# Performance work log

Measured on AMD Instinct MI355X. Metric: run time of the kernel, lower is better.

## Reference

```python
import jax, jax.numpy as jnp
import numpy as np
from jax import lax


def setup_inputs() -> dict:
    key = jax.random.key(0)
    k1, k2 = jax.random.split(key)
    L, B, d = 2048, 16, 1024
    x = jax.random.normal(k1, (L, B, d), dtype=jnp.float32)
    val_range = (3.0 / d) ** 0.5
    weight = jax.random.uniform(k2, (d, 3 * d), dtype=jnp.float32,
                                minval=-val_range, maxval=val_range)
    bias = jnp.zeros((2 * d,), dtype=jnp.float32)
    c0 = jnp.zeros((B, d), dtype=jnp.float32)
    return {"x": x, "weight": weight, "bias": bias, "c0": c0}


def reference(x, weight, bias, c0):
    # x: [L, B, d]; weight: [d, 3d]; bias: [2d]; c0: [B, d]
    L, B, d = x.shape
    u = (x.reshape(-1, d) @ weight).reshape(L, B, d, 3)
    x_tilde = u[..., 0]                               # [L, B, d]
    forget = jax.nn.sigmoid(u[..., 1] + bias[:d])     # [L, B, d]
    reset = jax.nn.sigmoid(u[..., 2] + bias[d:])      # [L, B, d]
    # k == 3 case: x_prime is the raw input (highway connection)
    x_prime = x

    def step(c_prev, ft_xt):
        ft, xt = ft_xt
        c = (c_prev - xt) * ft + xt
        return c, c

    c_last, cs = lax.scan(step, c0, (forget, x_tilde))
    g = jnp.tanh(cs)  # activation_type == 1
    h = (g - x_prime) * reset + x_prime
    return h, c_last
```

## Files before the change

kernel.cpp:

```cpp
#include <hip/hip_runtime.h>

#define L_SEQ 2048
#define BATCH 16
#define DDIM  1024
#define MDIM  (L_SEQ * BATCH)
#define NDIM  (3 * DDIM)
#define KDIM  DDIM
#define CH    (BATCH * DDIM)
#define NSEG  32
#define SEGL  64

typedef __attribute__((ext_vector_type(8))) short short8;
typedef __attribute__((ext_vector_type(4))) float f32x4;

static __device__ __forceinline__ unsigned short f2bf(float f) {
  unsigned int u = __builtin_bit_cast(unsigned int, f);
  unsigned int lsb = (u >> 16) & 1u;
  u += 0x7fffu + lsb;
  return (unsigned short)(u >> 16);
}
static __device__ __forceinline__ float bf2f(unsigned short s) {
  unsigned int u = ((unsigned int)s) << 16;
  return __builtin_bit_cast(float, u);
}

static __device__ __forceinline__ void gll16(const void* g, void* l) {
  __builtin_amdgcn_global_load_lds(
      (const __attribute__((address_space(1))) unsigned int*)g,
      (__attribute__((address_space(3))) unsigned int*)l, 16, 0, 0);
}


__global__ void k_convert_x(const float4* __restrict__ x, ushort4* __restrict__ xb, int n4) {
  int i = blockIdx.x * blockDim.x + threadIdx.x;
  int stride = gridDim.x * blockDim.x;
  for (; i < n4; i += stride) {
    float4 v = x[i];
    ushort4 o;
    o.x = f2bf(v.x); o.y = f2bf(v.y); o.z = f2bf(v.z); o.w = f2bf(v.w);
    xb[i] = o;
  }
}

__global__ void k_convert_w(const float* __restrict__ w, unsigned short* __restrict__ wb) {
  int gid = blockIdx.x * 256 + threadIdx.x;
  int k = gid & (KDIM - 1);
  int n = gid >> 10;
  int col = (n < DDIM) ? 3 * n : (n < 2 * DDIM) ? 3 * (n - DDIM) + 1 : 3 * (n - 2 * DDIM) + 2;
  wb[gid] = f2bf(w[(size_t)k * NDIM + col]);
}


#define MFMA1(I, J, A, B) \
  acc[I][J] = __builtin_amdgcn_mfma_f32_16x16x32_bf16(A, B, acc[I][J], 0, 0, 0);

#define MFMAQ(BASE)                                   \
  MFMA1(BASE + 0, 0, aa0, bb0) MFMA1(BASE + 0, 1, aa0, bb1) \
  MFMA1(BASE + 0, 2, aa0, bb2) MFMA1(BASE + 0, 3, aa0, bb3) \
  MFMA1(BASE + 1, 0, aa1, bb0) MFMA1(BASE + 1, 1, aa1, bb1) \
  MFMA1(BASE + 1, 2, aa1, bb2) MFMA1(BASE + 1, 3, aa1, bb3) \
  MFMA1(BASE + 2, 0, aa2, bb0) MFMA1(BASE + 2, 1, aa2, bb1) \
  MFMA1(BASE + 2, 2, aa2, bb2) MFMA1(BASE + 2, 3, aa2, bb3) \
  MFMA1(BASE + 3, 0, aa3, bb0) MFMA1(BASE + 3, 1, aa3, bb1) \
  MFMA1(BASE + 3, 2, aa3, bb2) MFMA1(BASE + 3, 3, aa3, bb3)

#define PH_BAR() __builtin_amdgcn_s_barrier()

#define VM_WAIT4() asm volatile("s_waitcnt vmcnt(4)" ::: "memory")

#define TILE64(T) do {                                                        \
  const char* bufC = LDSc + ((T) & 1) * 65536;                                \
  char*       bufN = LDSc + (((T) + 1) & 1) * 65536;                          \
  const int stA = (((T) + 1) & 15) * 128;                                     \
                 \
  aa0 = *(const short8*)(bufC + aRd);                                         \
  aa1 = *(const short8*)(bufC + aRd + 1024);                                  \
  aa2 = *(const short8*)(bufC + aRd + 2048);                                  \
  aa3 = *(const short8*)(bufC + aRd + 3072);                                  \
  bb0 = *(const short8*)(bufC + 32768 + bRd);                                 \
  bb1 = *(const short8*)(bufC + 32768 + bRd + 1024);                          \
  bb2 = *(const short8*)(bufC + 32768 + bRd + 2048);                          \
  bb3 = *(const short8*)(bufC + 32768 + bRd + 3072);                          \
  gll16(srcA0 + stA, bufN + dstOff);                                          \
  gll16(srcA1 + stA, bufN + 8192 + dstOff);                                   \
  PH_BAR();                                                                   \
  __builtin_amdgcn_s_setprio(1); MFMAQ(0) __builtin_amdgcn_s_setprio(0);      \
  PH_BAR();                                                                   \
              \
  aa0 = *(const short8*)(bufC + aRd + 4096);                                  \
  aa1 = *(const short8*)(bufC + aRd + 5120);                                  \
  aa2 = *(const short8*)(bufC + aRd + 6144);                                  \
  aa3 = *(const short8*)(bufC + aRd + 7168);                                  \
  gll16(srcB0 + stA, bufN + 32768 + dstOff);                                  \
  gll16(srcB1 + stA, bufN + 40960 + dstOff);                                  \
  PH_BAR();                                                                   \
  __builtin_amdgcn_s_setprio(1); MFMAQ(4) __builtin_amdgcn_s_setprio(0);      \
  VM_WAIT4();                                                                 \
  PH_BAR();                                                                   \
                 \
  aa0 = *(const short8*)(bufC + 16384 + aRd);                                 \
  aa1 = *(const short8*)(bufC + 16384 + aRd + 1024);                          \
  aa2 = *(const short8*)(bufC + 16384 + aRd + 2048);                          \
  aa3 = *(const short8*)(bufC + 16384 + aRd + 3072);                          \
  bb0 = *(const short8*)(bufC + 49152 + bRd);                                 \
  bb1 = *(const short8*)(bufC + 49152 + bRd + 1024);                          \
  bb2 = *(const short8*)(bufC + 49152 + bRd + 2048);                          \
  bb3 = *(const short8*)(bufC + 49152 + bRd + 3072);                          \
  gll16(srcA0 + stA + 64, bufN + 16384 + dstOff);                             \
  gll16(srcA1 + stA + 64, bufN + 24576 + dstOff);                             \
  PH_BAR();                                                                   \
  __builtin_amdgcn_s_setprio(1); MFMAQ(0) __builtin_amdgcn_s_setprio(0);      \
  PH_BAR();                                                                   \
              \
  aa0 = *(const short8*)(bufC + 16384 + aRd + 4096);                          \
  aa1 = *(const short8*)(bufC + 16384 + aRd + 5120);                          \
  aa2 = *(const short8*)(bufC + 16384 + aRd + 6144);                          \
  aa3 = *(const short8*)(bufC + 16384 + aRd + 7168);                          \
  gll16(srcB0 + stA + 64, bufN + 49152 + dstOff);                             \
  gll16(srcB1 + stA + 64, bufN + 57344 + dstOff);                             \
  PH_BAR();                                                                   \
  __builtin_amdgcn_s_setprio(1); MFMAQ(4) __builtin_amdgcn_s_setprio(0);      \
  VM_WAIT4();                                                                 \
  PH_BAR();                                                                   \
} while (0)

__global__ __launch_bounds__(512, 2) void k_gemm256(
    const unsigned short* __restrict__ xb,
    const unsigned short* __restrict__ wb,
    const float* __restrict__ bias,
    unsigned short* __restrict__ xtb,
    unsigned short* __restrict__ fbuf,
    unsigned short* __restrict__ rbuf) {
  __shared__ char LDS[131072];
  char* LDSc = LDS;

  const int tid  = threadIdx.x;
  const int lane = tid & 63;
  const int wid  = tid >> 6;
  const int wr   = wid >> 2;
  const int wc   = wid & 3;

  int bid = blockIdx.x;
  int wg = (bid & 7) * 192 + (bid >> 3);
  int mt = wg / 12;
  int nt = wg - mt * 12;
  const int rowBase = mt * 256;
  const int colBase = nt * 256;

  const int l15 = lane & 15;
  const int sl  = lane >> 4;
  const int ra0 = wr * 128 + l15;
  const int rb0 = wc * 64 + l15;
  const int aRd = ra0 * 64 + (sl ^ ((ra0 >> 1) & 3)) * 16;
  const int bRd = rb0 * 64 + (sl ^ ((rb0 >> 1) & 3)) * 16;

  const int p0i = tid, p1i = 512 + tid;
  const int r0 = p0i >> 2, r1 = p1i >> 2;
  const int s0 = (p0i & 3) ^ ((r0 >> 1) & 3);
  const int s1 = (p1i & 3) ^ ((r1 >> 1) & 3);
  const char* srcA0 = (const char*)xb + (size_t)(rowBase + r0) * 2048 + s0 * 16;
  const char* srcA1 = (const char*)xb + (size_t)(rowBase + r1) * 2048 + s1 * 16;
  const char* srcB0 = (const char*)wb + (size_t)(colBase + r0) * 2048 + s0 * 16;
  const char* srcB1 = (const char*)wb + (size_t)(colBase + r1) * 2048 + s1 * 16;
  const int dstOff = wid * 1024;

  f32x4 acc[8][4];
#pragma unroll
  for (int ii = 0; ii < 8; ++ii)
#pragma unroll
    for (int jj = 0; jj < 4; ++jj)
      acc[ii][jj] = (f32x4){0.f, 0.f, 0.f, 0.f};

  gll16(srcA0, LDSc + dstOff);
  gll16(srcA1, LDSc + 8192 + dstOff);
  gll16(srcB0, LDSc + 32768 + dstOff);
  gll16(srcB1, LDSc + 40960 + dstOff);
  gll16(srcA0 + 64, LDSc + 16384 + dstOff);
  gll16(srcA1 + 64, LDSc + 24576 + dstOff);
  gll16(srcB0 + 64, LDSc + 49152 + dstOff);
  gll16(srcB1 + 64, LDSc + 57344 + dstOff);
  asm volatile("s_waitcnt vmcnt(0)" ::: "memory");
  __builtin_amdgcn_s_barrier();

  short8 aa0, aa1, aa2, aa3;
  short8 bb0, bb1, bb2, bb3;

  for (int i = 0; i < 8; ++i) {
    TILE64(2 * i);
    TILE64(2 * i + 1);
  }
  asm volatile("s_waitcnt vmcnt(0)" ::: "memory");

  const int region = colBase >> 10;
#pragma unroll
  for (int qm = 0; qm < 2; ++qm) {
#pragma unroll
    for (int m = 0; m < 4; ++m) {
      int grow = rowBase + wr * 128 + qm * 64 + m * 16 + ((lane >> 4) << 2);
#pragma unroll
      for (int n = 0; n < 4; ++n) {
        int gcol = colBase + wc * 64 + n * 16 + (lane & 15);
        f32x4 v = acc[qm * 4 + m][n];
        if (region == 0) {
#pragma unroll
          for (int j = 0; j < 4; ++j)
            xtb[(size_t)(grow + j) * DDIM + gcol] = f2bf(v[j]);
        } else {
          float bv = bias[gcol - DDIM];
          unsigned short* dst = (region == 1) ? fbuf : rbuf;
          int lcol = gcol - (region << 10);
#pragma unroll
          for (int j = 0; j < 4; ++j) {
            float sg = 1.0f / (1.0f + __expf(-(v[j] + bv)));
            dst[(size_t)(grow + j) * DDIM + lcol] = f2bf(sg);
          }
        }
      }
    }
  }
}


__global__ __launch_bounds__(256) void k_scan1(
    const unsigned short* __restrict__ fbuf,
    const unsigned short* __restrict__ xtb,
    float4* __restrict__ AB) {
  int chp = blockIdx.x * 256 + threadIdx.x;
  int seg = blockIdx.y;
  size_t base = (size_t)seg * SEGL * CH + chp * 2;
  const unsigned int* fp = (const unsigned int*)(fbuf + base);
  const unsigned int* xp = (const unsigned int*)(xtb + base);
  float a0 = 1.f, a1 = 1.f, b0 = 0.f, b1 = 0.f;
#pragma unroll 8
  for (int s = 0; s < SEGL; ++s) {
    unsigned int fv = fp[(size_t)s * (CH / 2)];
    unsigned int xv = xp[(size_t)s * (CH / 2)];
    float f0 = bf2f((unsigned short)fv), f1 = bf2f((unsigned short)(fv >> 16));
    float x0 = bf2f((unsigned short)xv), x1 = bf2f((unsigned short)(xv >> 16));
    b0 = (b0 - x0) * f0 + x0;  a0 *= f0;
    b1 = (b1 - x1) * f1 + x1;  a1 *= f1;
  }
  AB[(size_t)seg * (CH / 2) + chp] = (float4){a0, b0, a1, b1};
}


__global__ __launch_bounds__(256) void k_scan2(
    const float* __restrict__ c0,
    const float4* __restrict__ AB,
    float* __restrict__ Cin,
    float* __restrict__ clast) {
  int chp = blockIdx.x * 256 + threadIdx.x;
  float2 cc = ((const float2*)c0)[chp];
  float ca = cc.x, cb = cc.y;
#pragma unroll
  for (int s = 0; s < NSEG; ++s) {
    ((float2*)Cin)[(size_t)s * (CH / 2) + chp] = (float2){ca, cb};
    float4 ab = AB[(size_t)s * (CH / 2) + chp];
    ca = ca * ab.x + ab.y;
    cb = cb * ab.z + ab.w;
  }
  ((float2*)clast)[chp] = (float2){ca, cb};
}


__global__ __launch_bounds__(256) void k_scan3(
    const float* __restrict__ x,
    const unsigned short* __restrict__ fbuf,
    const unsigned short* __restrict__ xtb,
    const unsigned short* __restrict__ rbuf,
    const float* __restrict__ Cin,
    float* __restrict__ h) {
  int chp = blockIdx.x * 256 + threadIdx.x;
  int seg = blockIdx.y;
  float2 cc = ((const float2*)Cin)[(size_t)seg * (CH / 2) + chp];
  float ca = cc.x, cb = cc.y;
  size_t base = (size_t)seg * SEGL * CH + chp * 2;
  const unsigned int* fp = (const unsigned int*)(fbuf + base);
  const unsigned int* tp = (const unsigned int*)(xtb + base);
  const unsigned int* rp = (const unsigned int*)(rbuf + base);
  const float2* xp = (const float2*)(x + base);
  float2* hp = (float2*)(h + base);
#pragma unroll 4
  for (int s = 0; s < SEGL; ++s) {
    unsigned int fv = fp[(size_t)s * (CH / 2)];
    unsigned int tv = tp[(size_t)s * (CH / 2)];
    unsigned int rv = rp[(size_t)s * (CH / 2)];
    float2 xv = xp[(size_t)s * (CH / 2)];
    float f0 = bf2f((unsigned short)fv), f1 = bf2f((unsigned short)(fv >> 16));
    float t0 = bf2f((unsigned short)tv), t1 = bf2f((unsigned short)(tv >> 16));
    float r0 = bf2f((unsigned short)rv), r1 = bf2f((unsigned short)(rv >> 16));
    ca = (ca - t0) * f0 + t0;
    cb = (cb - t1) * f1 + t1;
    float e0 = __expf(-2.f * fabsf(ca));
    float e1 = __expf(-2.f * fabsf(cb));
    float g0 = copysignf((1.f - e0) / (1.f + e0), ca);
    float g1 = copysignf((1.f - e1) / (1.f + e1), cb);
    float h0 = (g0 - xv.x) * r0 + xv.x;
    float h1 = (g1 - xv.y) * r1 + xv.y;
    hp[(size_t)s * (CH / 2)] = (float2){h0, h1};
  }
}


extern "C" void kernel_launch(void* const* d_in, const int* in_sizes, int n_in,
                              void* d_out, int out_size, void* d_ws, size_t ws_size,
                              hipStream_t stream) {
  const float* x    = (const float*)d_in[0];
  const float* w    = (const float*)d_in[1];
  const float* bias = (const float*)d_in[2];
  const float* c0   = (const float*)d_in[3];
  float* out = (float*)d_out;
  char* ws = (char*)d_ws;

  unsigned short* wb   = (unsigned short*)(ws);
  float4*         AB   = (float4*)(ws);
  float*          Cin  = (float*)(ws + 4194304);
  unsigned short* xtb  = (unsigned short*)(ws + 6291456);
  unsigned short* fbuf = (unsigned short*)(ws + 73400320);
  unsigned short* rbuf = (unsigned short*)(ws + 140509184);
  unsigned short* xb = (unsigned short*)d_out;

  k_convert_x<<<2048, 256, 0, stream>>>((const float4*)x, (ushort4*)xb, MDIM * KDIM / 4);
  k_convert_w<<<(NDIM * KDIM) / 256, 256, 0, stream>>>(w, wb);

  k_gemm256<<<1536, 512, 0, stream>>>(xb, wb, bias, xtb, fbuf, rbuf);

  k_scan1<<<dim3(32, NSEG), 256, 0, stream>>>(fbuf, xtb, AB);
  k_scan2<<<32, 256, 0, stream>>>(c0, AB, Cin, out + (size_t)L_SEQ * CH);
  k_scan3<<<dim3(32, NSEG), 256, 0, stream>>>(x, fbuf, xtb, rbuf, Cin, out);
}
```

Before: 407.2 us.

## Restructure GEMM k-tile loop: issue all prefetches upfront, drop per-phase barriers

Each k-tile iteration now issues all eight global-to-LDS prefetches for the next tile at the start, then runs four MFMA quadrants with register double-buffered operand fragments, interleaving LDS reads with MFMA work. The four barrier pairs and partial vmcnt waits per tile are replaced by a single vmcnt(0) wait and one barrier at the end. This removes synchronization overhead and lets waves drift relative to each other. In exchange it raises register pressure (16 operand fragments live) under the 2-wave-per-SIMD launch bound, and a full vmcnt(0) wait at tile end may expose global load latency.

Measured after the change: 426.2 us. 4.7% more time.

```diff
diff --git a/kernel.cpp b/kernel.cpp
--- a/kernel.cpp
+++ b/kernel.cpp
@@ -54,74 +54,68 @@
 #define MFMA1(I, J, A, B) \
   acc[I][J] = __builtin_amdgcn_mfma_f32_16x16x32_bf16(A, B, acc[I][J], 0, 0, 0);
 
-#define MFMAQ(BASE)                                   \
-  MFMA1(BASE + 0, 0, aa0, bb0) MFMA1(BASE + 0, 1, aa0, bb1) \
-  MFMA1(BASE + 0, 2, aa0, bb2) MFMA1(BASE + 0, 3, aa0, bb3) \
-  MFMA1(BASE + 1, 0, aa1, bb0) MFMA1(BASE + 1, 1, aa1, bb1) \
-  MFMA1(BASE + 1, 2, aa1, bb2) MFMA1(BASE + 1, 3, aa1, bb3) \
-  MFMA1(BASE + 2, 0, aa2, bb0) MFMA1(BASE + 2, 1, aa2, bb1) \
-  MFMA1(BASE + 2, 2, aa2, bb2) MFMA1(BASE + 2, 3, aa2, bb3) \
-  MFMA1(BASE + 3, 0, aa3, bb0) MFMA1(BASE + 3, 1, aa3, bb1) \
-  MFMA1(BASE + 3, 2, aa3, bb2) MFMA1(BASE + 3, 3, aa3, bb3)
-
-#define PH_BAR() __builtin_amdgcn_s_barrier()
-
-#define VM_WAIT4() asm volatile("s_waitcnt vmcnt(4)" ::: "memory")
+#define MFMAQ(BASE, A0, A1, A2, A3, B0, B1, B2, B3)      \
+  MFMA1(BASE + 0, 0, A0, B0) MFMA1(BASE + 0, 1, A0, B1)  \
+  MFMA1(BASE + 0, 2, A0, B2) MFMA1(BASE + 0, 3, A0, B3)  \
+  MFMA1(BASE + 1, 0, A1, B0) MFMA1(BASE + 1, 1, A1, B1)  \
+  MFMA1(BASE + 1, 2, A1, B2) MFMA1(BASE + 1, 3, A1, B3)  \
+  MFMA1(BASE + 2, 0, A2, B0) MFMA1(BASE + 2, 1, A2, B1)  \
+  MFMA1(BASE + 2, 2, A2, B2) MFMA1(BASE + 2, 3, A2, B3)  \
+  MFMA1(BASE + 3, 0, A3, B0) MFMA1(BASE + 3, 1, A3, B1)  \
+  MFMA1(BASE + 3, 2, A3, B2) MFMA1(BASE + 3, 3, A3, B3)
 
 #define TILE64(T) do {                                                        \
   const char* bufC = LDSc + ((T) & 1) * 65536;                                \
   char*       bufN = LDSc + (((T) + 1) & 1) * 65536;                          \
   const int stA = (((T) + 1) & 15) * 128;                                     \
-                 \
-  aa0 = *(const short8*)(bufC + aRd);                                         \
-  aa1 = *(const short8*)(bufC + aRd + 1024);                                  \
-  aa2 = *(const short8*)(bufC + aRd + 2048);                                  \
-  aa3 = *(const short8*)(bufC + aRd + 3072);                                  \
-  bb0 = *(const short8*)(bufC + 32768 + bRd);                                 \
-  bb1 = *(const short8*)(bufC + 32768 + bRd + 1024);                          \
-  bb2 = *(const short8*)(bufC + 32768 + bRd + 2048);                          \
-  bb3 = *(const short8*)(bufC + 32768 + bRd + 3072);                          \
+         \
   gll16(srcA0 + stA, bufN + dstOff);                                          \
   gll16(srcA1 + stA, bufN + 8192 + dstOff);                                   \
-  PH_BAR();                                                                   \
-  __builtin_amdgcn_s_setprio(1); MFMAQ(0) __builtin_amdgcn_s_setprio(0);      \
-  PH_BAR();                                                                   \
-              \
-  aa0 = *(const short8*)(bufC + aRd + 4096);                                  \
-  aa1 = *(const short8*)(bufC + aRd + 5120);                                  \
-  aa2 = *(const short8*)(bufC + aRd + 6144);                                  \
-  aa3 = *(const short8*)(bufC + aRd + 7168);                                  \
   gll16(srcB0 + stA, bufN + 32768 + dstOff);                                  \
   gll16(srcB1 + stA, bufN + 40960 + dstOff);                                  \
-  PH_BAR();                                                                   \
-  __builtin_amdgcn_s_setprio(1); MFMAQ(4) __builtin_amdgcn_s_setprio(0);      \
-  VM_WAIT4();                                                                 \
-  PH_BAR();                                                                   \
-                 \
-  aa0 = *(const short8*)(bufC + 16384 + aRd);                                 \
-  aa1 = *(const short8*)(bufC + 16384 + aRd + 1024);                          \
-  aa2 = *(const short8*)(bufC + 16384 + aRd + 2048);                          \
-  aa3 = *(const short8*)(bufC + 16384 + aRd + 3072);                          \
-  bb0 = *(const short8*)(bufC + 49152 + bRd);                                 \
-  bb1 = *(const short8*)(bufC + 49152 + bRd + 1024);                          \
-  bb2 = *(const short8*)(bufC + 49152 + bRd + 2048);                          \
-  bb3 = *(const short8*)(bufC + 49152 + bRd + 3072);                          \
   gll16(srcA0 + stA + 64, bufN + 16384 + dstOff);                             \
   gll16(srcA1 + stA + 64, bufN + 24576 + dstOff);                             \
-  PH_BAR();                                                                   \
-  __builtin_amdgcn_s_setprio(1); MFMAQ(0) __builtin_amdgcn_s_setprio(0);      \
-  PH_BAR();                                                                   \
-              \
-  aa0 = *(const short8*)(bufC + 16384 + aRd + 4096);                          \
-  aa1 = *(const short8*)(bufC + 16384 + aRd + 5120);                          \
-  aa2 = *(const short8*)(bufC + 16384 + aRd + 6144);                          \
-  aa3 = *(const short8*)(bufC + 16384 + aRd + 7168);                          \
   gll16(srcB0 + stA + 64, bufN + 49152 + dstOff);                             \
   gll16(srcB1 + stA + 64, bufN + 57344 + dstOff);                             \
-  PH_BAR();                                                                   \
-  __builtin_amdgcn_s_setprio(1); MFMAQ(4) __builtin_amdgcn_s_setprio(0);      \
-  VM_WAIT4();                                                                 \
-  PH_BAR();                                                                   \
+  __builtin_amdgcn_sched_barrier(0);                                          \
+      \
+  a0 = *(const short8*)(bufC + aRd);                                          \
+  a1 = *(const short8*)(bufC + aRd + 1024);                                   \
+  a2 = *(const short8*)(bufC + aRd + 2048);                                   \
+  a3 = *(const short8*)(bufC + aRd + 3072);                                   \
+  b0 = *(const short8*)(bufC + 32768 + bRd);                                  \
+  b1 = *(const short8*)(bufC + 32768 + bRd + 1024);                           \
+  b2 = *(const short8*)(bufC + 32768 + bRd + 2048);                           \
+  b3 = *(const short8*)(bufC + 32768 + bRd + 3072);                           \
+  na0 = *(const short8*)(bufC + aRd + 4096);                                  \
+  na1 = *(const short8*)(bufC + aRd + 5120);                                  \
+  na2 = *(const short8*)(bufC + aRd + 6144);                                  \
+  na3 = *(const short8*)(bufC + aRd + 7168);                                  \
+  __builtin_amdgcn_s_setprio(1);                                              \
+  MFMAQ(0, a0, a1, a2, a3, b0, b1, b2, b3)                                    \
+  __builtin_amdgcn_s_setprio(0);                                              \
+  a0 = *(const short8*)(bufC + 16384 + aRd);                                  \
+  a1 = *(const short8*)(bufC + 16384 + aRd + 1024);                           \
+  a2 = *(const short8*)(bufC + 16384 + aRd + 2048);                           \
+  a3 = *(const short8*)(bufC + 16384 + aRd + 3072);                           \
+  nb0 = *(const short8*)(bufC + 49152 + bRd);                                 \
+  nb1 = *(const short8*)(bufC + 49152 + bRd + 1024);                          \
+  nb2 = *(const short8*)(bufC + 49152 + bRd + 2048);                          \
+  nb3 = *(const short8*)(bufC + 49152 + bRd + 3072);                          \
+  __builtin_amdgcn_s_setprio(1);                                              \
+  MFMAQ(4, na0, na1, na2, na3, b0, b1, b2, b3)                                \
+  __builtin_amdgcn_s_setprio(0);                                              \
+  na0 = *(const short8*)(bufC + 16384 + aRd + 4096);                          \
+  na1 = *(const short8*)(bufC + 16384 + aRd + 5120);                          \
+  na2 = *(const short8*)(bufC + 16384 + aRd + 6144);                          \
+  na3 = *(const short8*)(bufC + 16384 + aRd + 7168);                          \
+  __builtin_amdgcn_s_setprio(1);                                              \
+  MFMAQ(0, a0, a1, a2, a3, nb0, nb1, nb2, nb3)                                \
+  MFMAQ(4, na0, na1, na2, na3, nb0, nb1, nb2, nb3)                            \
+  __builtin_amdgcn_s_setprio(0);                                              \
+          \
+  asm volatile("s_waitcnt vmcnt(0)" ::: "memory");                            \
+  __builtin_amdgcn_s_barrier();                                               \
 } while (0)
 
 __global__ __launch_bounds__(512, 2) void k_gemm256(
@@ -182,14 +176,13 @@
   asm volatile("s_waitcnt vmcnt(0)" ::: "memory");
   __builtin_amdgcn_s_barrier();
 
-  short8 aa0, aa1, aa2, aa3;
-  short8 bb0, bb1, bb2, bb3;
+  short8 a0, a1, a2, a3, na0, na1, na2, na3;
+  short8 b0, b1, b2, b3, nb0, nb1, nb2, nb3;
 
   for (int i = 0; i < 8; ++i) {
     TILE64(2 * i);
     TILE64(2 * i + 1);
   }
-  asm volatile("s_waitcnt vmcnt(0)" ::: "memory");
 
   const int region = colBase >> 10;
 #pragma unroll
```
